# Performance work log

Measured on AMD Instinct MI355X. Metric: run time of the kernel, lower is better.

Reference implementation:

```python
import jax, jax.numpy as jnp
import numpy as np

NUM_EXPERTS = 64
TOP_K = 8
ALPHA = 0.001


def setup_inputs() -> dict:
    key = jax.random.key(0)
    k1, k2 = jax.random.split(key)
    hidden_states = jax.random.normal(k1, (16384, 2048), dtype=jnp.float32)
    # nn.Linear(D, E) weight has shape (E, D); init ~ N(0, 1/sqrt(D))
    weight = jax.random.normal(k2, (NUM_EXPERTS, 2048), dtype=jnp.float32) / jnp.sqrt(2048.0)
    return {"hidden_states": hidden_states, "weight": weight}


def reference(hidden_states, weight):
    # Router logits: (N, E)
    logits = jnp.einsum("nd,ed->ne", hidden_states, weight)
    scores = jax.nn.softmax(logits, axis=-1)

    # top-k (lax.top_k returns sorted values; torch used sorted=False, same set)
    topk_weights, topk_indices = jax.lax.top_k(scores, TOP_K)  # (N, K)
    topk_weights = topk_weights / jnp.sum(topk_weights, axis=-1, keepdims=True)

    # Aux load-balancing loss (training path). Instead of materializing a
    # (N, K, E) one-hot tensor, count tokens per expert with a scatter-add.
    num_tokens = hidden_states.shape[0]
    counts = jnp.zeros((NUM_EXPERTS,), dtype=jnp.float32).at[topk_indices.ravel()].add(1.0)
    tokens_per_expert = counts / (num_tokens * TOP_K)
    mean_prob = jnp.mean(scores, axis=0)  # (E,)
    aux_loss = ALPHA * NUM_EXPERTS * jnp.sum(tokens_per_expert * mean_prob)

    return topk_weights, topk_indices, aux_loss
```

## Files before the change

### kernel.cpp

```cpp
#include <hip/hip_runtime.h>
#include <hip/hip_bf16.h>

#define N_TOKENS 16384
#define DIM      2048
#define NEXP     64
#define TOPK     8
#define LOSCALE  2048.0f
#define NBLOCKS  512
#define LSTRIDE  66

typedef _Float16 half8   __attribute__((ext_vector_type(8)));
typedef float    floatx4 __attribute__((ext_vector_type(4)));

__global__ __launch_bounds__(256) void wprep_kernel(const float* __restrict__ W,
                                                    _Float16* __restrict__ Whi,
                                                    _Float16* __restrict__ Wlo) {
    int i = blockIdx.x * 256 + threadIdx.x;
    float w = W[i];
    _Float16 h = (_Float16)w;
    Whi[i] = h;
    Wlo[i] = (_Float16)((w - (float)h) * LOSCALE);
}

__global__ __launch_bounds__(256) void moe_kernel(const float* __restrict__ A,
                                                  const _Float16* __restrict__ Whi,
                                                  const _Float16* __restrict__ Wlo,
                                                  float* __restrict__ out_w,
                                                  float* __restrict__ out_i,
                                                  float* __restrict__ out_aux,
                                                  float* __restrict__ cnt_ws,
                                                  float* __restrict__ sp_ws,
                                                  unsigned int* __restrict__ ticket) {
    __shared__ float lds[4 * 32 * LSTRIDE];
    __shared__ float s_cnt[NEXP];
    __shared__ float s_sp[NEXP];
    __shared__ int   s_last;

    const int lane  = threadIdx.x & 63;
    const int wv    = threadIdx.x >> 6;
    const int row16 = lane & 15;
    const int quad  = lane >> 4;
    const int tbase = blockIdx.x * 32;
    const int kbase = wv * 512;

    if (threadIdx.x < NEXP) { s_cnt[threadIdx.x] = 0.f; s_sp[threadIdx.x] = 0.f; }

    floatx4 acc0[2][4] = {};
    floatx4 acc1[2][4] = {};

    const float* ap0 = A + (size_t)(tbase + row16) * DIM + quad * 8;
    const float* ap1 = ap0 + (size_t)16 * DIM;
    const size_t boff = (size_t)row16 * DIM + quad * 8;

    float4 ar[2][2];
    half8  bh[4], bl[4];
    ar[0][0] = *(const float4*)(ap0 + kbase);
    ar[0][1] = *(const float4*)(ap0 + kbase + 4);
    ar[1][0] = *(const float4*)(ap1 + kbase);
    ar[1][1] = *(const float4*)(ap1 + kbase + 4);
    #pragma unroll
    for (int nt = 0; nt < 4; ++nt) {
        bh[nt] = *(const half8*)(Whi + (size_t)nt * 16 * DIM + boff + kbase);
        bl[nt] = *(const half8*)(Wlo + (size_t)nt * 16 * DIM + boff + kbase);
    }

    for (int it = 0; it < 16; ++it) {
        float4 arn[2][2];
        half8  bhn[4], bln[4];
        if (it < 15) {
            int kc = kbase + (it + 1) * 32;
            arn[0][0] = *(const float4*)(ap0 + kc);
            arn[0][1] = *(const float4*)(ap0 + kc + 4);
            arn[1][0] = *(const float4*)(ap1 + kc);
            arn[1][1] = *(const float4*)(ap1 + kc + 4);
            #pragma unroll
            for (int nt = 0; nt < 4; ++nt) {
                bhn[nt] = *(const half8*)(Whi + (size_t)nt * 16 * DIM + boff + kc);
                bln[nt] = *(const half8*)(Wlo + (size_t)nt * 16 * DIM + boff + kc);
            }
        }

        half8 ah[2], al[2];
        #pragma unroll
        for (int mt = 0; mt < 2; ++mt) {
            float av[8] = {ar[mt][0].x, ar[mt][0].y, ar[mt][0].z, ar[mt][0].w,
                           ar[mt][1].x, ar[mt][1].y, ar[mt][1].z, ar[mt][1].w};
            #pragma unroll
            for (int j = 0; j < 8; ++j) {
                _Float16 h = (_Float16)av[j];
                ah[mt][j] = h;
                al[mt][j] = (_Float16)((av[j] - (float)h) * LOSCALE);
            }
        }

        #pragma unroll
        for (int mt = 0; mt < 2; ++mt)
            #pragma unroll
            for (int nt = 0; nt < 4; ++nt) {
                acc0[mt][nt] = __builtin_amdgcn_mfma_f32_16x16x32_f16(ah[mt], bh[nt], acc0[mt][nt], 0, 0, 0);
                acc1[mt][nt] = __builtin_amdgcn_mfma_f32_16x16x32_f16(ah[mt], bl[nt], acc1[mt][nt], 0, 0, 0);
                acc1[mt][nt] = __builtin_amdgcn_mfma_f32_16x16x32_f16(al[mt], bh[nt], acc1[mt][nt], 0, 0, 0);
            }

        #pragma unroll
        for (int mt = 0; mt < 2; ++mt) { ar[mt][0] = arn[mt][0]; ar[mt][1] = arn[mt][1]; }
        #pragma unroll
        for (int nt = 0; nt < 4; ++nt) { bh[nt] = bhn[nt]; bl[nt] = bln[nt]; }
    }

    const float inv = 1.0f / LOSCALE;
    #pragma unroll
    for (int mt = 0; mt < 2; ++mt)
        #pragma unroll
        for (int nt = 0; nt < 4; ++nt)
            #pragma unroll
            for (int reg = 0; reg < 4; ++reg) {
                int tok = mt * 16 + quad * 4 + reg;
                lds[(wv * 32 + tok) * LSTRIDE + nt * 16 + row16] =
                    acc0[mt][nt][reg] + acc1[mt][nt][reg] * inv;
            }
    __syncthreads();

    float sp = 0.f, cnt = 0.f;
    for (int i = 0; i < 8; ++i) {
        int t = wv * 8 + i;
        float lg = (lds[t * LSTRIDE + lane]              + lds[(32 + t) * LSTRIDE + lane])
                 + (lds[(64 + t) * LSTRIDE + lane]       + lds[(96 + t) * LSTRIDE + lane]);

        float m = lg;
        #pragma unroll
        for (int off = 32; off; off >>= 1) m = fmaxf(m, __shfl_xor(m, off));
        float e = expf(lg - m);
        float ssum = e;
        #pragma unroll
        for (int off = 32; off; off >>= 1) ssum += __shfl_xor(ssum, off);
        float score = e / ssum;
        sp += score;

        int rank = 0;
        #pragma unroll
        for (int j = 0; j < 64; ++j) {
            float sj = __shfl(score, j);
            rank += (sj > score) || (sj == score && j < lane);
        }
        bool sel = rank < TOPK;

        float v = sel ? score : 0.f;
        #pragma unroll
        for (int off = 32; off; off >>= 1) v += __shfl_xor(v, off);

        if (sel) {
            out_w[(size_t)(tbase + t) * TOPK + rank] = score / v;
            out_i[(size_t)(tbase + t) * TOPK + rank] = (float)lane;
            cnt += 1.f;
        }
    }

    atomicAdd(&s_sp[lane], sp);
    atomicAdd(&s_cnt[lane], cnt);
    __syncthreads();
    if (threadIdx.x < 64)       atomicAdd(&cnt_ws[threadIdx.x], s_cnt[threadIdx.x]);
    else if (threadIdx.x < 128) atomicAdd(&sp_ws[threadIdx.x - 64], s_sp[threadIdx.x - 64]);

    __threadfence();
    __syncthreads();
    if (threadIdx.x == 0)
        s_last = (atomicAdd(ticket, 1u) == (unsigned)(gridDim.x - 1));
    __syncthreads();
    if (s_last && threadIdx.x < 64) {
        float c = atomicAdd(&cnt_ws[threadIdx.x], 0.f);
        float p = atomicAdd(&sp_ws[threadIdx.x], 0.f);
        float v = (c / (float)(N_TOKENS * TOPK)) * (p / (float)N_TOKENS);
        #pragma unroll
        for (int off = 32; off; off >>= 1) v += __shfl_xor(v, off);
        if (threadIdx.x == 0) out_aux[0] = 0.001f * (float)NEXP * v;
    }
}

extern "C" void kernel_launch(void* const* d_in, const int* in_sizes, int n_in,
                              void* d_out, int out_size, void* d_ws, size_t ws_size,
                              hipStream_t stream) {
    const float* A = (const float*)d_in[0];
    const float* W = (const float*)d_in[1];
    float* out = (float*)d_out;

    _Float16*     whi    = (_Float16*)d_ws;
    _Float16*     wlo    = whi + (size_t)NEXP * DIM;
    float*        cnt_ws = (float*)(wlo + (size_t)NEXP * DIM);
    float*        sp_ws  = cnt_ws + NEXP;
    unsigned int* ticket = (unsigned int*)(sp_ws + NEXP);

    hipMemsetAsync(cnt_ws, 0, 2 * NEXP * sizeof(float) + sizeof(unsigned int), stream);

    hipLaunchKernelGGL(wprep_kernel, dim3(NEXP * DIM / 256), dim3(256), 0, stream,
                       W, whi, wlo);

    float* out_w = out;
    float* out_i = out + (size_t)N_TOKENS * TOPK;
    float* out_a = out + 2 * (size_t)N_TOKENS * TOPK;

    hipLaunchKernelGGL(moe_kernel, dim3(NBLOCKS), dim3(256), 0, stream,
                       A, whi, wlo, out_w, out_i, out_a, cnt_ws, sp_ws, ticket);
}
```

Measured before the change: 256.7 us.

## Split K across eight waves per block and replicate global atomic counters

Doubles the block to 512 threads (eight waves), each wave covering a 256-wide K slab instead of 512, so each wave runs half as many MFMA iterations and more waves are resident to hide memory latency. The LDS cross-wave reduction now sums eight partial logits and each wave handles four tokens in the epilogue. Global expert counters are replicated 32 ways by block index to reduce atomic contention, and the last block sums the replicas. This costs a larger LDS footprint and higher register pressure under the 512-thread launch bound, and the workspace memset grows.

```diff
diff --git a/kernel.cpp b/kernel.cpp
--- a/kernel.cpp
+++ b/kernel.cpp
@@ -7,7 +7,11 @@
 #define TOPK     8
 #define LOSCALE  2048.0f
 #define NBLOCKS  512
+#define NWAVES   8
+#define KSLAB    256
+#define NCHUNK   8
 #define LSTRIDE  66
+#define NREP     32
 
 typedef _Float16 half8   __attribute__((ext_vector_type(8)));
 typedef float    floatx4 __attribute__((ext_vector_type(4)));
@@ -22,16 +26,16 @@
     Wlo[i] = (_Float16)((w - (float)h) * LOSCALE);
 }
 
-__global__ __launch_bounds__(256) void moe_kernel(const float* __restrict__ A,
-                                                  const _Float16* __restrict__ Whi,
-                                                  const _Float16* __restrict__ Wlo,
-                                                  float* __restrict__ out_w,
-                                                  float* __restrict__ out_i,
-                                                  float* __restrict__ out_aux,
-                                                  float* __restrict__ cnt_ws,
-                                                  float* __restrict__ sp_ws,
-                                                  unsigned int* __restrict__ ticket) {
-    __shared__ float lds[4 * 32 * LSTRIDE];
+__global__ __launch_bounds__(512, 4) void moe_kernel(const float* __restrict__ A,
+                                                     const _Float16* __restrict__ Whi,
+                                                     const _Float16* __restrict__ Wlo,
+                                                     float* __restrict__ out_w,
+                                                     float* __restrict__ out_i,
+                                                     float* __restrict__ out_aux,
+                                                     float* __restrict__ cnt_ws,
+                                                     float* __restrict__ sp_ws,
+                                                     unsigned int* __restrict__ ticket) {
+    __shared__ float lds[NWAVES * 32 * LSTRIDE];
     __shared__ float s_cnt[NEXP];
     __shared__ float s_sp[NEXP];
     __shared__ int   s_last;
@@ -41,7 +45,7 @@
     const int row16 = lane & 15;
     const int quad  = lane >> 4;
     const int tbase = blockIdx.x * 32;
-    const int kbase = wv * 512;
+    const int kbase = wv * KSLAB;
 
     if (threadIdx.x < NEXP) { s_cnt[threadIdx.x] = 0.f; s_sp[threadIdx.x] = 0.f; }
 
@@ -64,10 +68,10 @@
         bl[nt] = *(const half8*)(Wlo + (size_t)nt * 16 * DIM + boff + kbase);
     }
 
-    for (int it = 0; it < 16; ++it) {
+    for (int it = 0; it < NCHUNK; ++it) {
         float4 arn[2][2];
         half8  bhn[4], bln[4];
-        if (it < 15) {
+        if (it < NCHUNK - 1) {
             int kc = kbase + (it + 1) * 32;
             arn[0][0] = *(const float4*)(ap0 + kc);
             arn[0][1] = *(const float4*)(ap0 + kc + 4);
@@ -122,10 +126,13 @@
     __syncthreads();
 
     float sp = 0.f, cnt = 0.f;
-    for (int i = 0; i < 8; ++i) {
-        int t = wv * 8 + i;
-        float lg = (lds[t * LSTRIDE + lane]              + lds[(32 + t) * LSTRIDE + lane])
-                 + (lds[(64 + t) * LSTRIDE + lane]       + lds[(96 + t) * LSTRIDE + lane]);
+    for (int i = 0; i < 4; ++i) {
+        int t = wv * 4 + i;
+        float lg01 = lds[t * LSTRIDE + lane]         + lds[(32 + t) * LSTRIDE + lane];
+        float lg23 = lds[(64 + t) * LSTRIDE + lane]  + lds[(96 + t) * LSTRIDE + lane];
+        float lg45 = lds[(128 + t) * LSTRIDE + lane] + lds[(160 + t) * LSTRIDE + lane];
+        float lg67 = lds[(192 + t) * LSTRIDE + lane] + lds[(224 + t) * LSTRIDE + lane];
+        float lg = (lg01 + lg23) + (lg45 + lg67);
 
         float m = lg;
         #pragma unroll
@@ -159,8 +166,9 @@
     atomicAdd(&s_sp[lane], sp);
     atomicAdd(&s_cnt[lane], cnt);
     __syncthreads();
-    if (threadIdx.x < 64)       atomicAdd(&cnt_ws[threadIdx.x], s_cnt[threadIdx.x]);
-    else if (threadIdx.x < 128) atomicAdd(&sp_ws[threadIdx.x - 64], s_sp[threadIdx.x - 64]);
+    const int rep = (blockIdx.x & (NREP - 1)) * NEXP;
+    if (threadIdx.x < 64)       atomicAdd(&cnt_ws[rep + threadIdx.x], s_cnt[threadIdx.x]);
+    else if (threadIdx.x < 128) atomicAdd(&sp_ws[rep + threadIdx.x - 64], s_sp[threadIdx.x - 64]);
 
     __threadfence();
     __syncthreads();
@@ -168,8 +176,12 @@
         s_last = (atomicAdd(ticket, 1u) == (unsigned)(gridDim.x - 1));
     __syncthreads();
     if (s_last && threadIdx.x < 64) {
-        float c = atomicAdd(&cnt_ws[threadIdx.x], 0.f);
-        float p = atomicAdd(&sp_ws[threadIdx.x], 0.f);
+        float c = 0.f, p = 0.f;
+        #pragma unroll
+        for (int r = 0; r < NREP; ++r) {
+            c += atomicAdd(&cnt_ws[r * NEXP + threadIdx.x], 0.f);
+            p += atomicAdd(&sp_ws [r * NEXP + threadIdx.x], 0.f);
+        }
         float v = (c / (float)(N_TOKENS * TOPK)) * (p / (float)N_TOKENS);
         #pragma unroll
         for (int off = 32; off; off >>= 1) v += __shfl_xor(v, off);
@@ -187,10 +199,10 @@
     _Float16*     whi    = (_Float16*)d_ws;
     _Float16*     wlo    = whi + (size_t)NEXP * DIM;
     float*        cnt_ws = (float*)(wlo + (size_t)NEXP * DIM);
-    float*        sp_ws  = cnt_ws + NEXP;
-    unsigned int* ticket = (unsigned int*)(sp_ws + NEXP);
-
-    hipMemsetAsync(cnt_ws, 0, 2 * NEXP * sizeof(float) + sizeof(unsigned int), stream);
+    float*        sp_ws  = cnt_ws + (size_t)NREP * NEXP;
+    unsigned int* ticket = (unsigned int*)(sp_ws + (size_t)NREP * NEXP);
+
+    hipMemsetAsync(cnt_ws, 0, 2 * NREP * NEXP * sizeof(float) + sizeof(unsigned int), stream);
 
     hipLaunchKernelGGL(wprep_kernel, dim3(NEXP * DIM / 256), dim3(256), 0, stream,
                        W, whi, wlo);
@@ -199,6 +211,6 @@
     float* out_i = out + (size_t)N_TOKENS * TOPK;
     float* out_a = out + 2 * (size_t)N_TOKENS * TOPK;
 
-    hipLaunchKernelGGL(moe_kernel, dim3(NBLOCKS), dim3(256), 0, stream,
+    hipLaunchKernelGGL(moe_kernel, dim3(NBLOCKS), dim3(512), 0, stream,
                        A, whi, wlo, out_w, out_i, out_a, cnt_ws, sp_ws, ticket);
 }
```

After: 338.9 us. 1.32x slower.

## Double-buffer K-loop register prefetch and replicate global atomic accumulators

Applied to the files above, without the earlier changes.

The K loop now keeps two register sets in flight, issuing loads two iterations ahead while the other set is consumed, so more memory latency is hidden than with the single-stage prefetch. Separately, the per-expert count and probability-sum atomics are spread across 32 replicas keyed by block index, which reduces contention on the same global addresses. The last block then sums all replicas. This costs more registers, which may lower occupancy, and a larger memset.

```diff
diff --git a/kernel.cpp b/kernel.cpp
--- a/kernel.cpp
+++ b/kernel.cpp
@@ -8,6 +8,7 @@
 #define LOSCALE  2048.0f
 #define NBLOCKS  512
 #define LSTRIDE  66
+#define NREP     32
 
 typedef _Float16 half8   __attribute__((ext_vector_type(8)));
 typedef float    floatx4 __attribute__((ext_vector_type(4)));
@@ -48,64 +49,59 @@
     floatx4 acc0[2][4] = {};
     floatx4 acc1[2][4] = {};
 
-    const float* ap0 = A + (size_t)(tbase + row16) * DIM + quad * 8;
+    const float* ap0 = A + (size_t)(tbase + row16) * DIM + quad * 8 + kbase;
     const float* ap1 = ap0 + (size_t)16 * DIM;
-    const size_t boff = (size_t)row16 * DIM + quad * 8;
-
-    float4 ar[2][2];
-    half8  bh[4], bl[4];
-    ar[0][0] = *(const float4*)(ap0 + kbase);
-    ar[0][1] = *(const float4*)(ap0 + kbase + 4);
-    ar[1][0] = *(const float4*)(ap1 + kbase);
-    ar[1][1] = *(const float4*)(ap1 + kbase + 4);
+    const size_t boff = (size_t)row16 * DIM + quad * 8 + kbase;
+
+    float4 ar0[2][2], ar1[2][2];
+    half8  bh0[4], bl0[4], bh1[4], bl1[4];
+
+#define LOADSET(AR, BH, BL, KC)                                               \
+    do {                                                                      \
+        AR[0][0] = *(const float4*)(ap0 + (KC));                              \
+        AR[0][1] = *(const float4*)(ap0 + (KC) + 4);                          \
+        AR[1][0] = *(const float4*)(ap1 + (KC));                              \
+        AR[1][1] = *(const float4*)(ap1 + (KC) + 4);                          \
+        _Pragma("unroll")                                                     \
+        for (int _nt = 0; _nt < 4; ++_nt) {                                   \
+            BH[_nt] = *(const half8*)(Whi + (size_t)_nt * 16 * DIM + boff + (KC)); \
+            BL[_nt] = *(const half8*)(Wlo + (size_t)_nt * 16 * DIM + boff + (KC)); \
+        }                                                                     \
+    } while (0)
+
+#define CONSUME(AR, BH, BL)                                                   \
+    do {                                                                      \
+        half8 _ah[2], _al[2];                                                 \
+        _Pragma("unroll")                                                     \
+        for (int _mt = 0; _mt < 2; ++_mt) {                                   \
+            float _av[8] = {AR[_mt][0].x, AR[_mt][0].y, AR[_mt][0].z, AR[_mt][0].w, \
+                            AR[_mt][1].x, AR[_mt][1].y, AR[_mt][1].z, AR[_mt][1].w};\
+            _Pragma("unroll")                                                 \
+            for (int _j = 0; _j < 8; ++_j) {                                  \
+                _Float16 _h = (_Float16)_av[_j];                              \
+                _ah[_mt][_j] = _h;                                            \
+                _al[_mt][_j] = (_Float16)((_av[_j] - (float)_h) * LOSCALE);   \
+            }                                                                 \
+        }                                                                     \
+        _Pragma("unroll")                                                     \
+        for (int _mt = 0; _mt < 2; ++_mt)                                     \
+            _Pragma("unroll")                                                 \
+            for (int _nt = 0; _nt < 4; ++_nt) {                               \
+                acc0[_mt][_nt] = __builtin_amdgcn_mfma_f32_16x16x32_f16(_ah[_mt], BH[_nt], acc0[_mt][_nt], 0, 0, 0); \
+                acc1[_mt][_nt] = __builtin_amdgcn_mfma_f32_16x16x32_f16(_ah[_mt], BL[_nt], acc1[_mt][_nt], 0, 0, 0); \
+                acc1[_mt][_nt] = __builtin_amdgcn_mfma_f32_16x16x32_f16(_al[_mt], BH[_nt], acc1[_mt][_nt], 0, 0, 0); \
+            }                                                                 \
+    } while (0)
+
+    LOADSET(ar0, bh0, bl0, 0);
+    LOADSET(ar1, bh1, bl1, 32);
+
     #pragma unroll
-    for (int nt = 0; nt < 4; ++nt) {
-        bh[nt] = *(const half8*)(Whi + (size_t)nt * 16 * DIM + boff + kbase);
-        bl[nt] = *(const half8*)(Wlo + (size_t)nt * 16 * DIM + boff + kbase);
-    }
-
-    for (int it = 0; it < 16; ++it) {
-        float4 arn[2][2];
-        half8  bhn[4], bln[4];
-        if (it < 15) {
-            int kc = kbase + (it + 1) * 32;
-            arn[0][0] = *(const float4*)(ap0 + kc);
-            arn[0][1] = *(const float4*)(ap0 + kc + 4);
-            arn[1][0] = *(const float4*)(ap1 + kc);
-            arn[1][1] = *(const float4*)(ap1 + kc + 4);
-            #pragma unroll
-            for (int nt = 0; nt < 4; ++nt) {
-                bhn[nt] = *(const half8*)(Whi + (size_t)nt * 16 * DIM + boff + kc);
-                bln[nt] = *(const half8*)(Wlo + (size_t)nt * 16 * DIM + boff + kc);
-            }
-        }
-
-        half8 ah[2], al[2];
-        #pragma unroll
-        for (int mt = 0; mt < 2; ++mt) {
-            float av[8] = {ar[mt][0].x, ar[mt][0].y, ar[mt][0].z, ar[mt][0].w,
-                           ar[mt][1].x, ar[mt][1].y, ar[mt][1].z, ar[mt][1].w};
-            #pragma unroll
-            for (int j = 0; j < 8; ++j) {
-                _Float16 h = (_Float16)av[j];
-                ah[mt][j] = h;
-                al[mt][j] = (_Float16)((av[j] - (float)h) * LOSCALE);
-            }
-        }
-
-        #pragma unroll
-        for (int mt = 0; mt < 2; ++mt)
-            #pragma unroll
-            for (int nt = 0; nt < 4; ++nt) {
-                acc0[mt][nt] = __builtin_amdgcn_mfma_f32_16x16x32_f16(ah[mt], bh[nt], acc0[mt][nt], 0, 0, 0);
-                acc1[mt][nt] = __builtin_amdgcn_mfma_f32_16x16x32_f16(ah[mt], bl[nt], acc1[mt][nt], 0, 0, 0);
-                acc1[mt][nt] = __builtin_amdgcn_mfma_f32_16x16x32_f16(al[mt], bh[nt], acc1[mt][nt], 0, 0, 0);
-            }
-
-        #pragma unroll
-        for (int mt = 0; mt < 2; ++mt) { ar[mt][0] = arn[mt][0]; ar[mt][1] = arn[mt][1]; }
-        #pragma unroll
-        for (int nt = 0; nt < 4; ++nt) { bh[nt] = bhn[nt]; bl[nt] = bln[nt]; }
+    for (int u = 0; u < 8; ++u) {
+        CONSUME(ar0, bh0, bl0);
+        if (u < 7) LOADSET(ar0, bh0, bl0, (2 * u + 2) * 32);
+        CONSUME(ar1, bh1, bl1);
+        if (u < 7) LOADSET(ar1, bh1, bl1, (2 * u + 3) * 32);
     }
 
     const float inv = 1.0f / LOSCALE;
@@ -159,8 +155,9 @@
     atomicAdd(&s_sp[lane], sp);
     atomicAdd(&s_cnt[lane], cnt);
     __syncthreads();
-    if (threadIdx.x < 64)       atomicAdd(&cnt_ws[threadIdx.x], s_cnt[threadIdx.x]);
-    else if (threadIdx.x < 128) atomicAdd(&sp_ws[threadIdx.x - 64], s_sp[threadIdx.x - 64]);
+    const int rep = (blockIdx.x & (NREP - 1)) * NEXP;
+    if (threadIdx.x < 64)       atomicAdd(&cnt_ws[rep + threadIdx.x], s_cnt[threadIdx.x]);
+    else if (threadIdx.x < 128) atomicAdd(&sp_ws[rep + threadIdx.x - 64], s_sp[threadIdx.x - 64]);
 
     __threadfence();
     __syncthreads();
@@ -168,8 +165,12 @@
         s_last = (atomicAdd(ticket, 1u) == (unsigned)(gridDim.x - 1));
     __syncthreads();
     if (s_last && threadIdx.x < 64) {
-        float c = atomicAdd(&cnt_ws[threadIdx.x], 0.f);
-        float p = atomicAdd(&sp_ws[threadIdx.x], 0.f);
+        float c = 0.f, p = 0.f;
+        #pragma unroll
+        for (int r = 0; r < NREP; ++r) {
+            c += atomicAdd(&cnt_ws[r * NEXP + threadIdx.x], 0.f);
+            p += atomicAdd(&sp_ws [r * NEXP + threadIdx.x], 0.f);
+        }
         float v = (c / (float)(N_TOKENS * TOPK)) * (p / (float)N_TOKENS);
         #pragma unroll
         for (int off = 32; off; off >>= 1) v += __shfl_xor(v, off);
@@ -187,10 +188,10 @@
     _Float16*     whi    = (_Float16*)d_ws;
     _Float16*     wlo    = whi + (size_t)NEXP * DIM;
     float*        cnt_ws = (float*)(wlo + (size_t)NEXP * DIM);
-    float*        sp_ws  = cnt_ws + NEXP;
-    unsigned int* ticket = (unsigned int*)(sp_ws + NEXP);
-
-    hipMemsetAsync(cnt_ws, 0, 2 * NEXP * sizeof(float) + sizeof(unsigned int), stream);
+    float*        sp_ws  = cnt_ws + (size_t)NREP * NEXP;
+    unsigned int* ticket = (unsigned int*)(sp_ws + (size_t)NREP * NEXP);
+
+    hipMemsetAsync(cnt_ws, 0, 2 * NREP * NEXP * sizeof(float) + sizeof(unsigned int), stream);
 
     hipLaunchKernelGGL(wprep_kernel, dim3(NEXP * DIM / 256), dim3(256), 0, stream,
                        W, whi, wlo);
```

New measurement: 257.7 us. No clear change (+0.4%).
